# Performance work log

Measured on AMD Instinct MI355X. Metric: run time of the kernel, lower is better.

## Reference

```python
import jax, jax.numpy as jnp
import numpy as np
from jax import lax

B, S, D, F = 2, 4096, 1024, 4096
LN_EPS = 1e-6

def _layer_norm(x, scale, bias):
    mu = jnp.mean(x, axis=-1, keepdims=True)
    var = jnp.mean(jnp.square(x - mu), axis=-1, keepdims=True)
    return (x - mu) * lax.rsqrt(var + LN_EPS) * scale + bias

def _gate_loop(q, k, v, a):
    # max-headed GateLoop: one head per channel, scalar complex state per channel
    # h_t = a_t * h_{t-1} + k_t * v_t ; y_t = q_t * h_t
    kv = (k * v).astype(jnp.complex64)
    def comb(e1, e2):
        a1, x1 = e1
        a2, x2 = e2
        return (a1 * a2, a2 * x1 + x2)
    _, h = lax.associative_scan(comb, (a, kv), axis=1)
    return q.astype(jnp.complex64) * h

def setup_inputs() -> dict:
    key = jax.random.key(0)
    ks = jax.random.split(key, 12)
    sd = 1.0 / np.sqrt(D)
    sf = 1.0 / np.sqrt(F)
    return {
        "x": jax.random.normal(ks[0], (B, S, D), jnp.float32),
        "Wq": jax.random.normal(ks[1], (D, D), jnp.float32) * sd,
        "Wk": jax.random.normal(ks[2], (D, D), jnp.float32) * sd,
        "Wv": jax.random.normal(ks[3], (D, D), jnp.float32) * sd,
        "Wa": jax.random.normal(ks[4], (D, 2 * D), jnp.float32) * sd,
        "Wg": jax.random.normal(ks[5], (D, D), jnp.float32) * sd,
        "Wo": jax.random.normal(ks[6], (D, D), jnp.float32) * sd,
        "ln1_scale": jnp.ones((D,), jnp.float32),
        "ln1_bias": jnp.zeros((D,), jnp.float32),
        "W1": jax.random.normal(ks[7], (D, F), jnp.float32) * sd,
        "b1": jax.random.normal(ks[8], (F,), jnp.float32) * 1e-6,
        "W2": jax.random.normal(ks[9], (F, D), jnp.float32) * sf,
        "b2": jax.random.normal(ks[10], (D,), jnp.float32) * 1e-6,
        "ln2_scale": jnp.ones((D,), jnp.float32),
        "ln2_bias": jnp.zeros((D,), jnp.float32),
    }

def reference(x, Wq, Wk, Wv, Wa, Wg, Wo, ln1_scale, ln1_bias, W1, b1, W2, b2, ln2_scale, ln2_bias):
    q = x @ Wq
    k = x @ Wk
    v = x @ Wv
    a = x @ Wa
    a_real, a_imag = jnp.split(a, 2, axis=-1)
    a_c = a_real + 1j * a_imag
    magnitude = jnp.abs(a_c)
    phase = jnp.angle(a_c)
    a_c = jax.nn.sigmoid(magnitude).astype(jnp.complex64) * jnp.exp(1j * phase)
    g = x.astype(jnp.complex64) @ Wg.astype(jnp.complex64)
    y = _gate_loop(q, k, v, a_c)
    y = y * (g * jax.nn.sigmoid(g))  # silu on complex g
    y = y @ Wo.astype(jnp.complex64)
    y = y.real
    # dropout deterministic (training=False)
    y = _layer_norm(y + x, ln1_scale, ln1_bias)
    h = jax.nn.gelu(y @ W1 + b1)
    out = h @ W2 + b2
    out = _layer_norm(out + y, ln2_scale, ln2_bias)
    return out
```

## Files before the change

kernel.cpp:

```cpp
#include <hip/hip_runtime.h>
#include <cstdint>

typedef unsigned short u16;
typedef unsigned int u32;

#define AS1 __attribute__((address_space(1)))
#define AS3 __attribute__((address_space(3)))

typedef _Float16 f16x8 __attribute__((ext_vector_type(8)));
typedef float f32x4 __attribute__((ext_vector_type(4)));

static constexpr int Bb = 2, Ss = 4096, Dd = 1024, Ff = 4096;
static constexpr int Mtok = Bb * Ss;
static constexpr int NCH = 128;
static constexpr int TCH = Ss / NCH;
static constexpr int PW = 6144;

__device__ __forceinline__ float h2f(u16 u) {
    union { u16 u; _Float16 h; } w; w.u = u; return (float)w.h;
}
__device__ __forceinline__ u16 f2h(float f) {
    union { _Float16 h; u16 u; } w; w.h = (_Float16)f; return w.u;
}

__device__ __forceinline__ void gload_lds16(const u16* g, u16* l) {
    __builtin_amdgcn_global_load_lds((const AS1 u32*)g, (AS3 u32*)l, 16, 0, 0);
}

__global__ __launch_bounds__(256) void cvt_f32_f16(const float* __restrict__ src,
                                                   u16* __restrict__ dst) {
    const long i = ((long)blockIdx.x * 256 + threadIdx.x) * 4;
    float4 f = *(const float4*)(src + i);
    ushort4 o;
    o.x = f2h(f.x); o.y = f2h(f.y); o.z = f2h(f.z); o.w = f2h(f.w);
    *(ushort4*)(dst + i) = o;
}

__global__ __launch_bounds__(1024) void transpose_f32_f16(const float* __restrict__ src,
                                                          u16* __restrict__ dst,
                                                          int K, int N) {
    __shared__ u16 t[32][33];
    const int tx = threadIdx.x, ty = threadIdx.y;
    const int n0 = blockIdx.x * 32, k0 = blockIdx.y * 32;
    t[ty][tx] = f2h(src[(long)(k0 + ty) * N + n0 + tx]);
    __syncthreads();
    dst[(long)(n0 + ty) * K + k0 + tx] = t[tx][ty];
}

template <int EPI>
__global__ __launch_bounds__(256, 2) void gemm_bt(const u16* __restrict__ A,
                                                  const u16* __restrict__ BT,
                                                  u16* __restrict__ C,
                                                  const float* __restrict__ bias,
                                                  int M, int N, int K,
                                                  int lda, int ldc) {
    __shared__ __align__(16) u16 sA[128 * 32];
    __shared__ __align__(16) u16 sB[128 * 32];
    const int tid = threadIdx.x;
    const int tm = blockIdx.y * 128;
    const int tn = blockIdx.x * 128;
    const int w = tid >> 6;
    const int lane = tid & 63;
    const int wm = (w >> 1) * 64;
    const int wn = (w & 1) * 64;
    const int q = lane >> 4;
    const int r16 = lane & 15;

    f32x4 acc[4][4];
#pragma unroll
    for (int i = 0; i < 4; i++)
#pragma unroll
        for (int j = 0; j < 4; j++) acc[i][j] = (f32x4){0.f, 0.f, 0.f, 0.f};

    const int s0 = tid, s1 = 256 + tid;
    const int row0 = s0 >> 2, kc0 = (s0 & 3) * 8;
    const int row1 = s1 >> 2, kc1 = (s1 & 3) * 8;
    const u16* Ar0 = A + (long)(tm + row0) * lda + kc0;
    const u16* Ar1 = A + (long)(tm + row1) * lda + kc1;
    const u16* Br0 = BT + (long)(tn + row0) * K + kc0;
    const u16* Br1 = BT + (long)(tn + row1) * K + kc1;

    const int kiters = K >> 5;
    for (int kt = 0; kt < kiters; ++kt) {
        const int ko = kt * 32;
        gload_lds16(Ar0 + ko, sA + s0 * 8);
        gload_lds16(Ar1 + ko, sA + s1 * 8);
        gload_lds16(Br0 + ko, sB + s0 * 8);
        gload_lds16(Br1 + ko, sB + s1 * 8);
        __syncthreads();
        f16x8 af[4], bfr[4];
#pragma unroll
        for (int mi = 0; mi < 4; mi++)
            af[mi] = *(const f16x8*)(sA + (wm + mi * 16 + r16) * 32 + q * 8);
#pragma unroll
        for (int ni = 0; ni < 4; ni++)
            bfr[ni] = *(const f16x8*)(sB + (wn + ni * 16 + r16) * 32 + q * 8);
#pragma unroll
        for (int mi = 0; mi < 4; mi++)
#pragma unroll
            for (int ni = 0; ni < 4; ni++)
                acc[mi][ni] = __builtin_amdgcn_mfma_f32_16x16x32_f16(
                    af[mi], bfr[ni], acc[mi][ni], 0, 0, 0);
        __syncthreads();
    }

#pragma unroll
    for (int mi = 0; mi < 4; mi++) {
#pragma unroll
        for (int ni = 0; ni < 4; ni++) {
            const int gcol = tn + wn + ni * 16 + r16;
            float bv = 0.f;
            if (EPI) bv = bias[gcol];
#pragma unroll
            for (int j = 0; j < 4; j++) {
                const int grow = tm + wm + mi * 16 + q * 4 + j;
                float v = acc[mi][ni][j];
                if (EPI) v += bv;
                if (EPI == 1) {
                    float t = tanhf(0.7978845608028654f * (v + 0.044715f * v * v * v));
                    v = 0.5f * v * (1.0f + t);
                }
                C[(long)grow * ldc + gcol] = f2h(v);
            }
        }
    }
}

template <int EPI>
__global__ __launch_bounds__(512, 2) void gemm8p(const u16* __restrict__ A,
                                                 const u16* __restrict__ BT,
                                                 u16* __restrict__ C,
                                                 const float* __restrict__ bias,
                                                 int M, int N, int K,
                                                 int lda, int ldc) {
    extern __shared__ u16 lds[];
    const int tid = threadIdx.x;

    const int ntn = N >> 8;
    int bid = blockIdx.x;
    {
        const int cpx = gridDim.x >> 3;
        bid = (bid & 7) * cpx + (bid >> 3);
    }
    const int tm = (bid / ntn) << 8;
    const int tn = (bid % ntn) << 8;

    const int srow = tid >> 3;
    const int scol = ((tid & 7) ^ (srow & 7)) << 3;
    const u16* Abase = A + (long)(tm + srow) * lda + scol;
    const u16* Bbase = BT + (long)(tn + srow) * (long)K + scol;
    const long lda64 = (long)lda << 6;
    const long ldb64 = (long)K << 6;

    const int nt = K >> 6;

    auto stA = [&](u16* bufbase, int h, int kt) {
        u16* d = bufbase + h * 8192 + tid * 8;
        const u16* g = Abase + (long)(h * 128) * lda + (kt << 6);
        gload_lds16(g, d);
        gload_lds16(g + lda64, d + 4096);
    };
    auto stB = [&](u16* bufbase, int h, int kt) {
        u16* d = bufbase + 16384 + h * 8192 + tid * 8;
        const u16* g = Bbase + (long)(h * 128) * (long)K + (kt << 6);
        gload_lds16(g, d);
        gload_lds16(g + ldb64, d + 4096);
    };

    const int wid = tid >> 6, lane = tid & 63;
    const int r16 = lane & 15, q = lane >> 4;
    const int wm = (wid >> 2) * 128;
    const int wn = (wid & 3) * 64;
    const int r7 = r16 & 7;
    const int cx0 = (q ^ r7) << 3;
    const int cx1 = ((4 | q) ^ r7) << 3;
    const int aoff = (wm + r16) * 64;
    const int boff = 16384 + (wn + r16) * 64;

    f32x4 acc[8][4];
#pragma unroll
    for (int i = 0; i < 8; i++)
#pragma unroll
        for (int j = 0; j < 4; j++) acc[i][j] = (f32x4){0.f, 0.f, 0.f, 0.f};

    {
        const int t1 = nt > 1 ? 1 : 0;
        stA(lds, 0, 0);
        stA(lds, 1, 0);
        stB(lds, 0, 0);
        stB(lds, 1, 0);
        stB(lds + 32768, 0, t1);
        stB(lds + 32768, 1, t1);
    }

    for (int it = 0; it < nt; ++it) {
        u16* sb = lds + ((it & 1) << 15);
        u16* so = lds + (((it & 1) ^ 1) << 15);
        const int tA = (it + 1 < nt) ? it + 1 : nt - 1;
        const int tB = (it + 2 < nt) ? it + 2 : nt - 1;

        asm volatile("s_waitcnt vmcnt(4)" ::: "memory");
        __builtin_amdgcn_s_barrier();

        f16x8 vb[4][2];
#pragma unroll
        for (int ni = 0; ni < 4; ni++) {
            vb[ni][0] = *(const f16x8*)(sb + boff + ni * 1024 + cx0);
            vb[ni][1] = *(const f16x8*)(sb + boff + ni * 1024 + cx1);
        }

#pragma unroll
        for (int p = 0; p < 4; ++p) {
            f16x8 pa[2][2];
#pragma unroll
            for (int m2 = 0; m2 < 2; m2++) {
                pa[m2][0] = *(const f16x8*)(sb + aoff + (2 * p + m2) * 1024 + cx0);
                pa[m2][1] = *(const f16x8*)(sb + aoff + (2 * p + m2) * 1024 + cx1);
            }
            if (p == 0)      stA(so, 0, tA);
            else if (p == 1) stA(so, 1, tA);
            else if (p == 2) stB(sb, 0, tB);
            else             stB(sb, 1, tB);
            __builtin_amdgcn_s_barrier();
            asm volatile("s_waitcnt lgkmcnt(0)" ::: "memory");
            __builtin_amdgcn_s_setprio(1);
#pragma unroll
            for (int m2 = 0; m2 < 2; m2++)
#pragma unroll
                for (int ni = 0; ni < 4; ni++) {
                    acc[2 * p + m2][ni] = __builtin_amdgcn_mfma_f32_16x16x32_f16(
                        pa[m2][0], vb[ni][0], acc[2 * p + m2][ni], 0, 0, 0);
                    acc[2 * p + m2][ni] = __builtin_amdgcn_mfma_f32_16x16x32_f16(
                        pa[m2][1], vb[ni][1], acc[2 * p + m2][ni], 0, 0, 0);
                }
            __builtin_amdgcn_s_setprio(0);
            __builtin_amdgcn_s_barrier();
        }
    }

    asm volatile("s_waitcnt vmcnt(0)" ::: "memory");

#pragma unroll
    for (int mi = 0; mi < 8; mi++) {
#pragma unroll
        for (int ni = 0; ni < 4; ni++) {
            const int gcol = tn + wn + ni * 16 + r16;
            float bv = 0.f;
            if (EPI) bv = bias[gcol];
#pragma unroll
            for (int j = 0; j < 4; j++) {
                const int grow = tm + wm + mi * 16 + q * 4 + j;
                float v = acc[mi][ni][j];
                if (EPI) v += bv;
                if (EPI == 1) {
                    float t = tanhf(0.7978845608028654f * (v + 0.044715f * v * v * v));
                    v = 0.5f * v * (1.0f + t);
                }
                C[(long)grow * ldc + gcol] = f2h(v);
            }
        }
    }
}

__device__ __forceinline__ void a_transform(float ar, float ai, float& cr, float& ci) {
    float m = sqrtf(ar * ar + ai * ai);
    float sg = 1.f / (1.f + __expf(-m));
    float sc = sg / fmaxf(m, 1e-30f);
    cr = ar * sc;
    ci = ai * sc;
}

__global__ __launch_bounds__(1024) void scan1(const u16* __restrict__ pcat,
                                              float4* __restrict__ sum4) {
    const int b = blockIdx.y, c = blockIdx.x, d = threadIdx.x;
    float Arp = 1.f, Aip = 0.f, Xr = 0.f, Xi = 0.f;
    const long rowbase = (long)b * Ss + (long)c * TCH;
#pragma unroll 4
    for (int s = 0; s < TCH; ++s) {
        const long ro = (rowbase + s) * PW;
        float ar = h2f(pcat[ro + 3072 + d]);
        float ai = h2f(pcat[ro + 4096 + d]);
        float kk = h2f(pcat[ro + 1024 + d]);
        float vv = h2f(pcat[ro + 2048 + d]);
        float cr, ci;
        a_transform(ar, ai, cr, ci);
        float kv = kk * vv;
        float nXr = cr * Xr - ci * Xi + kv;
        float nXi = cr * Xi + ci * Xr;
        Xr = nXr; Xi = nXi;
        float nAr = cr * Arp - ci * Aip;
        float nAi = cr * Aip + ci * Arp;
        Arp = nAr; Aip = nAi;
    }
    sum4[((long)b * NCH + c) * 1024 + d] = make_float4(Arp, Aip, Xr, Xi);
}

__global__ __launch_bounds__(256) void scan2(const float4* __restrict__ sum4,
                                             float2* __restrict__ carry) {
    const int idx = blockIdx.x * 256 + threadIdx.x;
    const int b = idx >> 10, d = idx & 1023;
    float hr = 0.f, hi = 0.f;
    for (int cb = 0; cb < NCH / 8; ++cb) {
        float4 t[8];
#pragma unroll
        for (int j = 0; j < 8; j++)
            t[j] = sum4[((long)b * NCH + cb * 8 + j) * 1024 + d];
#pragma unroll
        for (int j = 0; j < 8; j++) {
            carry[((long)b * NCH + cb * 8 + j) * 1024 + d] = make_float2(hr, hi);
            float nr = t[j].x * hr - t[j].y * hi + t[j].z;
            float ni = t[j].x * hi + t[j].y * hr + t[j].w;
            hr = nr; hi = ni;
        }
    }
}

__global__ __launch_bounds__(1024) void scan3(u16* pcat,
                                              const float2* __restrict__ carry) {
    const int b = blockIdx.y, c = blockIdx.x, d = threadIdx.x;
    float2 h0 = carry[((long)b * NCH + c) * 1024 + d];
    float hr = h0.x, hi = h0.y;
    const long rowbase = (long)b * Ss + (long)c * TCH;
#pragma unroll 4
    for (int s = 0; s < TCH; ++s) {
        const long ro = (rowbase + s) * PW;
        float ar = h2f(pcat[ro + 3072 + d]);
        float ai = h2f(pcat[ro + 4096 + d]);
        float kk = h2f(pcat[ro + 1024 + d]);
        float vv = h2f(pcat[ro + 2048 + d]);
        float cr, ci;
        a_transform(ar, ai, cr, ci);
        float kv = kk * vv;
        float nhr = cr * hr - ci * hi + kv;
        float nhi = cr * hi + ci * hr;
        hr = nhr; hi = nhi;
        float gg = h2f(pcat[ro + 5120 + d]);
        float si = gg / (1.f + __expf(-gg));
        float yv = h2f(pcat[ro + d]) * hr * si;
        pcat[ro + d] = f2h(yv);
    }
}

template <int RESF32, int OUTF32>
__global__ __launch_bounds__(256) void ln_kernel(const u16* __restrict__ a, int sa,
                                                 const void* __restrict__ bres, int sres,
                                                 const float* __restrict__ scale,
                                                 const float* __restrict__ bias,
                                                 void* __restrict__ out, int sout) {
    const int row = blockIdx.x;
    const int tid = threadIdx.x;
    const long abase = (long)row * sa;
    const long rbase = (long)row * sres;
    const long obase = (long)row * sout;
    float v[4];
#pragma unroll
    for (int j = 0; j < 4; j++) {
        int d = tid * 4 + j;
        float rb = RESF32 ? ((const float*)bres)[rbase + d]
                          : h2f(((const u16*)bres)[rbase + d]);
        v[j] = h2f(a[abase + d]) + rb;
    }
    float s = v[0] + v[1] + v[2] + v[3];
    float s2 = v[0] * v[0] + v[1] * v[1] + v[2] * v[2] + v[3] * v[3];
#pragma unroll
    for (int off = 32; off; off >>= 1) {
        s += __shfl_down(s, off);
        s2 += __shfl_down(s2, off);
    }
    __shared__ float red[8];
    const int w = tid >> 6, lane = tid & 63;
    if (lane == 0) { red[w] = s; red[4 + w] = s2; }
    __syncthreads();
    if (tid == 0) {
        float ts = red[0] + red[1] + red[2] + red[3];
        float ts2 = red[4] + red[5] + red[6] + red[7];
        float mu = ts * (1.f / 1024.f);
        float var = ts2 * (1.f / 1024.f) - mu * mu;
        red[0] = mu;
        red[1] = rsqrtf(var + 1e-6f);
    }
    __syncthreads();
    const float mu = red[0], rs = red[1];
#pragma unroll
    for (int j = 0; j < 4; j++) {
        int d = tid * 4 + j;
        float y = (v[j] - mu) * rs * scale[d] + bias[d];
        if (OUTF32) ((float*)out)[obase + d] = y;
        else        ((u16*)out)[obase + d] = f2h(y);
    }
}

extern "C" void kernel_launch(void* const* d_in, const int* in_sizes, int n_in,
                              void* d_out, int out_size, void* d_ws, size_t ws_size,
                              hipStream_t stream) {
    const float* x    = (const float*)d_in[0];
    const float* Wq   = (const float*)d_in[1];
    const float* Wk   = (const float*)d_in[2];
    const float* Wv   = (const float*)d_in[3];
    const float* Wa   = (const float*)d_in[4];
    const float* Wg   = (const float*)d_in[5];
    const float* Wo   = (const float*)d_in[6];
    const float* ln1s = (const float*)d_in[7];
    const float* ln1b = (const float*)d_in[8];
    const float* W1   = (const float*)d_in[9];
    const float* b1   = (const float*)d_in[10];
    const float* W2   = (const float*)d_in[11];
    const float* b2   = (const float*)d_in[12];
    const float* ln2s = (const float*)d_in[13];
    const float* ln2b = (const float*)d_in[14];

    u16* ws    = (u16*)d_ws;
    u16* xb    = ws;
    u16* WTcat = xb + (8u << 20);
    u16* WTo   = WTcat + (6u << 20);
    u16* WT1   = WTo + (1u << 20);
    u16* WT2   = WT1 + (4u << 20);
    u16* pcat  = WT2 + (4u << 20);

    float4* sum4  = (float4*)WTcat;
    float2* carry = (float2*)(WTcat + (2u << 20));

    static bool attr_done = false;
    if (!attr_done) {
        hipFuncSetAttribute(reinterpret_cast<const void*>(&gemm8p<0>),
                            hipFuncAttributeMaxDynamicSharedMemorySize, 131072);
        hipFuncSetAttribute(reinterpret_cast<const void*>(&gemm8p<1>),
                            hipFuncAttributeMaxDynamicSharedMemorySize, 131072);
        attr_done = true;
    }


    cvt_f32_f16<<<dim3(8192), dim3(256), 0, stream>>>(x, xb);

    const dim3 tb(32, 32);
    transpose_f32_f16<<<dim3(32, 32), tb, 0, stream>>>(Wq, WTcat, 1024, 1024);
    transpose_f32_f16<<<dim3(32, 32), tb, 0, stream>>>(Wk, WTcat + (1u << 20), 1024, 1024);
    transpose_f32_f16<<<dim3(32, 32), tb, 0, stream>>>(Wv, WTcat + (2u << 20), 1024, 1024);
    transpose_f32_f16<<<dim3(64, 32), tb, 0, stream>>>(Wa, WTcat + (3u << 20), 1024, 2048);
    transpose_f32_f16<<<dim3(32, 32), tb, 0, stream>>>(Wg, WTcat + (5u << 20), 1024, 1024);
    transpose_f32_f16<<<dim3(32, 32), tb, 0, stream>>>(Wo, WTo, 1024, 1024);
    transpose_f32_f16<<<dim3(128, 32), tb, 0, stream>>>(W1, WT1, 1024, 4096);
    transpose_f32_f16<<<dim3(32, 128), tb, 0, stream>>>(W2, WT2, 4096, 1024);

    const dim3 gblk(256);
    gemm8p<0><<<dim3(768), dim3(512), 131072, stream>>>(xb, WTcat, pcat, nullptr,
                                                        Mtok, PW, 1024, 1024, PW);
    scan1<<<dim3(NCH, Bb), 1024, 0, stream>>>(pcat, sum4);
    scan2<<<dim3(8), 256, 0, stream>>>(sum4, carry);
    scan3<<<dim3(NCH, Bb), 1024, 0, stream>>>(pcat, carry);
    gemm_bt<0><<<dim3(8, 64), gblk, 0, stream>>>(pcat, WTo, pcat + 1024, nullptr,
                                                 Mtok, 1024, 1024, PW, PW);
    ln_kernel<1, 0><<<dim3(Mtok), gblk, 0, stream>>>(pcat + 1024, PW, x, 1024,
                                                     ln1s, ln1b, pcat, PW);
    gemm8p<1><<<dim3(512), dim3(512), 131072, stream>>>(pcat, WT1, pcat + 2048, b1,
                                                        Mtok, Ff, 1024, PW, PW);
    gemm_bt<2><<<dim3(8, 64), gblk, 0, stream>>>(pcat + 2048, WT2, pcat + 1024, b2,
                                                 Mtok, 1024, Ff, PW, PW);
    ln_kernel<0, 1><<<dim3(Mtok), gblk, 0, stream>>>(pcat + 1024, PW, pcat, PW,
                                                     ln2s, ln2b, d_out, 1024);
}
```

Baseline: 611.9 us.

## Replace simple 128x128 GEMM with pipelined 256x128 swizzled kernel for Wo and W2

Removes the basic single-buffered gemm_bt kernel and adds gemm8p_n128, a 512-thread, 256x128-tile variant of the pipelined gemm8p. It uses a double-buffered, XOR-swizzled LDS layout, 64-wide K steps, prefetch of future tiles and MFMA priority hints. It is used for the Wo projection and the W2 down projection, both with N=1024. The aim is to hide global load latency and cut LDS bank conflicts in those GEMMs, at the cost of fewer blocks (256) on a large GPU and more LDS per block.

```diff
diff --git a/kernel.cpp b/kernel.cpp
--- a/kernel.cpp
+++ b/kernel.cpp
@@ -45,85 +45,6 @@
     t[ty][tx] = f2h(src[(long)(k0 + ty) * N + n0 + tx]);
     __syncthreads();
     dst[(long)(n0 + ty) * K + k0 + tx] = t[tx][ty];
-}
-
-template <int EPI>
-__global__ __launch_bounds__(256, 2) void gemm_bt(const u16* __restrict__ A,
-                                                  const u16* __restrict__ BT,
-                                                  u16* __restrict__ C,
-                                                  const float* __restrict__ bias,
-                                                  int M, int N, int K,
-                                                  int lda, int ldc) {
-    __shared__ __align__(16) u16 sA[128 * 32];
-    __shared__ __align__(16) u16 sB[128 * 32];
-    const int tid = threadIdx.x;
-    const int tm = blockIdx.y * 128;
-    const int tn = blockIdx.x * 128;
-    const int w = tid >> 6;
-    const int lane = tid & 63;
-    const int wm = (w >> 1) * 64;
-    const int wn = (w & 1) * 64;
-    const int q = lane >> 4;
-    const int r16 = lane & 15;
-
-    f32x4 acc[4][4];
-#pragma unroll
-    for (int i = 0; i < 4; i++)
-#pragma unroll
-        for (int j = 0; j < 4; j++) acc[i][j] = (f32x4){0.f, 0.f, 0.f, 0.f};
-
-    const int s0 = tid, s1 = 256 + tid;
-    const int row0 = s0 >> 2, kc0 = (s0 & 3) * 8;
-    const int row1 = s1 >> 2, kc1 = (s1 & 3) * 8;
-    const u16* Ar0 = A + (long)(tm + row0) * lda + kc0;
-    const u16* Ar1 = A + (long)(tm + row1) * lda + kc1;
-    const u16* Br0 = BT + (long)(tn + row0) * K + kc0;
-    const u16* Br1 = BT + (long)(tn + row1) * K + kc1;
-
-    const int kiters = K >> 5;
-    for (int kt = 0; kt < kiters; ++kt) {
-        const int ko = kt * 32;
-        gload_lds16(Ar0 + ko, sA + s0 * 8);
-        gload_lds16(Ar1 + ko, sA + s1 * 8);
-        gload_lds16(Br0 + ko, sB + s0 * 8);
-        gload_lds16(Br1 + ko, sB + s1 * 8);
-        __syncthreads();
-        f16x8 af[4], bfr[4];
-#pragma unroll
-        for (int mi = 0; mi < 4; mi++)
-            af[mi] = *(const f16x8*)(sA + (wm + mi * 16 + r16) * 32 + q * 8);
-#pragma unroll
-        for (int ni = 0; ni < 4; ni++)
-            bfr[ni] = *(const f16x8*)(sB + (wn + ni * 16 + r16) * 32 + q * 8);
-#pragma unroll
-        for (int mi = 0; mi < 4; mi++)
-#pragma unroll
-            for (int ni = 0; ni < 4; ni++)
-                acc[mi][ni] = __builtin_amdgcn_mfma_f32_16x16x32_f16(
-                    af[mi], bfr[ni], acc[mi][ni], 0, 0, 0);
-        __syncthreads();
-    }
-
-#pragma unroll
-    for (int mi = 0; mi < 4; mi++) {
-#pragma unroll
-        for (int ni = 0; ni < 4; ni++) {
-            const int gcol = tn + wn + ni * 16 + r16;
-            float bv = 0.f;
-            if (EPI) bv = bias[gcol];
-#pragma unroll
-            for (int j = 0; j < 4; j++) {
-                const int grow = tm + wm + mi * 16 + q * 4 + j;
-                float v = acc[mi][ni][j];
-                if (EPI) v += bv;
-                if (EPI == 1) {
-                    float t = tanhf(0.7978845608028654f * (v + 0.044715f * v * v * v));
-                    v = 0.5f * v * (1.0f + t);
-                }
-                C[(long)grow * ldc + gcol] = f2h(v);
-            }
-        }
-    }
 }
 
 template <int EPI>
@@ -242,6 +163,142 @@
 
 #pragma unroll
     for (int mi = 0; mi < 8; mi++) {
+#pragma unroll
+        for (int ni = 0; ni < 4; ni++) {
+            const int gcol = tn + wn + ni * 16 + r16;
+            float bv = 0.f;
+            if (EPI) bv = bias[gcol];
+#pragma unroll
+            for (int j = 0; j < 4; j++) {
+                const int grow = tm + wm + mi * 16 + q * 4 + j;
+                float v = acc[mi][ni][j];
+                if (EPI) v += bv;
+                if (EPI == 1) {
+                    float t = tanhf(0.7978845608028654f * (v + 0.044715f * v * v * v));
+                    v = 0.5f * v * (1.0f + t);
+                }
+                C[(long)grow * ldc + gcol] = f2h(v);
+            }
+        }
+    }
+}
+
+template <int EPI>
+__global__ __launch_bounds__(512, 2) void gemm8p_n128(const u16* __restrict__ A,
+                                                      const u16* __restrict__ BT,
+                                                      u16* __restrict__ C,
+                                                      const float* __restrict__ bias,
+                                                      int M, int N, int K,
+                                                      int lda, int ldc) {
+    extern __shared__ u16 lds[];
+    const int tid = threadIdx.x;
+
+    const int ntn = N >> 7;
+    int bid = blockIdx.x;
+    {
+        const int cpx = gridDim.x >> 3;
+        bid = (bid & 7) * cpx + (bid >> 3);
+    }
+    const int tm = (bid / ntn) << 8;
+    const int tn = (bid % ntn) << 7;
+
+    const int srow = tid >> 3;
+    const int scol = ((tid & 7) ^ (srow & 7)) << 3;
+    const u16* Abase = A + (long)(tm + srow) * lda + scol;
+    const u16* Bbase = BT + (long)(tn + srow) * (long)K + scol;
+    const long lda64 = (long)lda << 6;
+    const long ldb64 = (long)K << 6;
+
+    const int nt = K >> 6;
+
+    auto stA = [&](u16* bufbase, int h, int kt) {
+        u16* d = bufbase + h * 8192 + tid * 8;
+        const u16* g = Abase + (long)(h * 128) * lda + (kt << 6);
+        gload_lds16(g, d);
+        gload_lds16(g + lda64, d + 4096);
+    };
+    auto stB = [&](u16* bufbase, int kt) {
+        u16* d = bufbase + 16384 + tid * 8;
+        const u16* g = Bbase + (kt << 6);
+        gload_lds16(g, d);
+        gload_lds16(g + ldb64, d + 4096);
+    };
+
+    const int wid = tid >> 6, lane = tid & 63;
+    const int r16 = lane & 15, q = lane >> 4;
+    const int wm = (wid >> 1) * 64;
+    const int wn = (wid & 1) * 64;
+    const int r7 = r16 & 7;
+    const int cx0 = (q ^ r7) << 3;
+    const int cx1 = ((4 | q) ^ r7) << 3;
+    const int aoff = (wm + r16) * 64;
+    const int boff = 16384 + (wn + r16) * 64;
+
+    f32x4 acc[4][4];
+#pragma unroll
+    for (int i = 0; i < 4; i++)
+#pragma unroll
+        for (int j = 0; j < 4; j++) acc[i][j] = (f32x4){0.f, 0.f, 0.f, 0.f};
+
+    {
+        const int t1 = nt > 1 ? 1 : 0;
+        stA(lds, 0, 0);
+        stA(lds, 1, 0);
+        stB(lds, 0);
+        stB(lds + 24576, t1);
+    }
+
+    for (int it = 0; it < nt; ++it) {
+        u16* sb = lds + (it & 1) * 24576;
+        u16* so = lds + ((it & 1) ^ 1) * 24576;
+        const int tA = (it + 1 < nt) ? it + 1 : nt - 1;
+        const int tB = (it + 2 < nt) ? it + 2 : nt - 1;
+
+        asm volatile("s_waitcnt vmcnt(2)" ::: "memory");
+        __builtin_amdgcn_s_barrier();
+
+        f16x8 vb[4][2];
+#pragma unroll
+        for (int ni = 0; ni < 4; ni++) {
+            vb[ni][0] = *(const f16x8*)(sb + boff + ni * 1024 + cx0);
+            vb[ni][1] = *(const f16x8*)(sb + boff + ni * 1024 + cx1);
+        }
+
+#pragma unroll
+        for (int p = 0; p < 2; ++p) {
+            f16x8 pa[2][2];
+#pragma unroll
+            for (int m2 = 0; m2 < 2; m2++) {
+                pa[m2][0] = *(const f16x8*)(sb + aoff + (2 * p + m2) * 1024 + cx0);
+                pa[m2][1] = *(const f16x8*)(sb + aoff + (2 * p + m2) * 1024 + cx1);
+            }
+            if (p == 0) {
+                stA(so, 0, tA);
+            } else {
+                stA(so, 1, tA);
+                stB(sb, tB);
+            }
+            __builtin_amdgcn_s_barrier();
+            asm volatile("s_waitcnt lgkmcnt(0)" ::: "memory");
+            __builtin_amdgcn_s_setprio(1);
+#pragma unroll
+            for (int m2 = 0; m2 < 2; m2++)
+#pragma unroll
+                for (int ni = 0; ni < 4; ni++) {
+                    acc[2 * p + m2][ni] = __builtin_amdgcn_mfma_f32_16x16x32_f16(
+                        pa[m2][0], vb[ni][0], acc[2 * p + m2][ni], 0, 0, 0);
+                    acc[2 * p + m2][ni] = __builtin_amdgcn_mfma_f32_16x16x32_f16(
+                        pa[m2][1], vb[ni][1], acc[2 * p + m2][ni], 0, 0, 0);
+                }
+            __builtin_amdgcn_s_setprio(0);
+            __builtin_amdgcn_s_barrier();
+        }
+    }
+
+    asm volatile("s_waitcnt vmcnt(0)" ::: "memory");
+
+#pragma unroll
+    for (int mi = 0; mi < 4; mi++) {
 #pragma unroll
         for (int ni = 0; ni < 4; ni++) {
             const int gcol = tn + wn + ni * 16 + r16;
@@ -426,6 +483,10 @@
                             hipFuncAttributeMaxDynamicSharedMemorySize, 131072);
         hipFuncSetAttribute(reinterpret_cast<const void*>(&gemm8p<1>),
                             hipFuncAttributeMaxDynamicSharedMemorySize, 131072);
+        hipFuncSetAttribute(reinterpret_cast<const void*>(&gemm8p_n128<0>),
+                            hipFuncAttributeMaxDynamicSharedMemorySize, 98304);
+        hipFuncSetAttribute(reinterpret_cast<const void*>(&gemm8p_n128<2>),
+                            hipFuncAttributeMaxDynamicSharedMemorySize, 98304);
         attr_done = true;
     }
 
@@ -442,20 +503,21 @@
     transpose_f32_f16<<<dim3(128, 32), tb, 0, stream>>>(W1, WT1, 1024, 4096);
     transpose_f32_f16<<<dim3(32, 128), tb, 0, stream>>>(W2, WT2, 4096, 1024);
 
-    const dim3 gblk(256);
     gemm8p<0><<<dim3(768), dim3(512), 131072, stream>>>(xb, WTcat, pcat, nullptr,
                                                         Mtok, PW, 1024, 1024, PW);
     scan1<<<dim3(NCH, Bb), 1024, 0, stream>>>(pcat, sum4);
     scan2<<<dim3(8), 256, 0, stream>>>(sum4, carry);
     scan3<<<dim3(NCH, Bb), 1024, 0, stream>>>(pcat, carry);
-    gemm_bt<0><<<dim3(8, 64), gblk, 0, stream>>>(pcat, WTo, pcat + 1024, nullptr,
-                                                 Mtok, 1024, 1024, PW, PW);
-    ln_kernel<1, 0><<<dim3(Mtok), gblk, 0, stream>>>(pcat + 1024, PW, x, 1024,
-                                                     ln1s, ln1b, pcat, PW);
+    gemm8p_n128<0><<<dim3(256), dim3(512), 98304, stream>>>(pcat, WTo, pcat + 1024,
+                                                            nullptr,
+                                                            Mtok, 1024, 1024, PW, PW);
+    ln_kernel<1, 0><<<dim3(Mtok), dim3(256), 0, stream>>>(pcat + 1024, PW, x, 1024,
+                                                          ln1s, ln1b, pcat, PW);
     gemm8p<1><<<dim3(512), dim3(512), 131072, stream>>>(pcat, WT1, pcat + 2048, b1,
                                                         Mtok, Ff, 1024, PW, PW);
-    gemm_bt<2><<<dim3(8, 64), gblk, 0, stream>>>(pcat + 2048, WT2, pcat + 1024, b2,
-                                                 Mtok, 1024, Ff, PW, PW);
-    ln_kernel<0, 1><<<dim3(Mtok), gblk, 0, stream>>>(pcat + 1024, PW, pcat, PW,
-                                                     ln2s, ln2b, d_out, 1024);
-}
+    gemm8p_n128<2><<<dim3(256), dim3(512), 98304, stream>>>(pcat + 2048, WT2,
+                                                            pcat + 1024, b2,
+                                                            Mtok, 1024, Ff, PW, PW);
+    ln_kernel<0, 1><<<dim3(Mtok), dim3(256), 0, stream>>>(pcat + 1024, PW, pcat, PW,
+                                                          ln2s, ln2b, d_out, 1024);
+}
```

Result: faster. 565.6 us (-7.6%).
